# Performance work log

Hardware: AMD Instinct MI355X
Metric: run time of the kernel (lower is better)

## Reference

```python
import jax, jax.numpy as jnp
import numpy as np

D_MODEL = 1024
N_HEADS = 16
D_K = D_MODEL // N_HEADS

def setup_inputs() -> dict:
    key = jax.random.key(0)
    ks = jax.random.split(key, 9)
    s = 1.0 / np.sqrt(D_MODEL)
    inp = {"x": jax.random.normal(ks[0], (2, 2048, D_MODEL), dtype=jnp.float32)}
    for i, name in enumerate(["q", "k", "v", "o"]):
        inp[f"W{name}"] = jax.random.uniform(ks[1 + i], (D_MODEL, D_MODEL), dtype=jnp.float32, minval=-s, maxval=s)
        inp[f"b{name}"] = jax.random.uniform(ks[5 + i], (D_MODEL,), dtype=jnp.float32, minval=-s, maxval=s)
    return inp

def _split_heads(t):
    B, S, _ = t.shape
    return t.reshape(B, S, N_HEADS, D_K).transpose(0, 2, 1, 3)  # [B,H,S,d_k]

def reference(x, Wq, bq, Wk, bk, Wv, bv, Wo, bo):
    # QKV projections (torch Linear: x @ W.T + b)
    q = _split_heads(x @ Wq.T + bq)
    k = _split_heads(x @ Wk.T + bk)
    v = _split_heads(x @ Wv.T + bv)
    scores = jnp.einsum('bhqd,bhkd->bhqk', q, k) / jnp.sqrt(jnp.asarray(D_K, x.dtype))
    probs = jax.nn.softmax(scores, axis=-1)
    attn = jnp.einsum('bhqk,bhkd->bhqd', probs, v)  # [B,H,S,d_k]
    B, H, S, _ = attn.shape
    merged = attn.transpose(0, 2, 1, 3).reshape(B, S, D_MODEL)
    return merged @ Wo.T + bo
```

## Files before the change

kernel.cpp:

```cpp
#include <hip/hip_runtime.h>
#include <hip/hip_bf16.h>
#include <stdint.h>


#define LOG2E 1.4426950408889634f

typedef float f32x4 __attribute__((ext_vector_type(4)));
typedef short bf16x8 __attribute__((ext_vector_type(8)));
typedef short bf16x4 __attribute__((ext_vector_type(4)));

__device__ __forceinline__ unsigned short f2bf(float f) {
  __hip_bfloat16 h = __float2bfloat16(f);
  return reinterpret_cast<unsigned short&>(h);
}

#define GLDS(g, l) __builtin_amdgcn_global_load_lds(                          \
    (const __attribute__((address_space(1))) void*)(g),                       \
    (__attribute__((address_space(3))) void*)(l), 16, 0, 0)

__global__ __launch_bounds__(256) void k_conv(const float* __restrict__ src,
                                              unsigned short* __restrict__ dst,
                                              int n4, float scale) {
  int i = blockIdx.x * 256 + threadIdx.x;
  const int stride = gridDim.x * 256;
  for (; i < n4; i += stride) {
    float4 v = ((const float4*)src)[i];
    ushort4 o;
    o.x = f2bf(v.x * scale);
    o.y = f2bf(v.y * scale);
    o.z = f2bf(v.z * scale);
    o.w = f2bf(v.w * scale);
    ((ushort4*)dst)[i] = o;
  }
}

__global__ __launch_bounds__(256) void k_convW(const float* __restrict__ wq,
                                               const float* __restrict__ wk,
                                               const float* __restrict__ wv,
                                               const float* __restrict__ wo,
                                               unsigned short* __restrict__ dq,
                                               unsigned short* __restrict__ dk,
                                               unsigned short* __restrict__ dv,
                                               unsigned short* __restrict__ dw) {
  const int m = blockIdx.y;
  const float* src = (m == 0) ? wq : (m == 1) ? wk : (m == 2) ? wv : wo;
  unsigned short* dst = (m == 0) ? dq : (m == 1) ? dk : (m == 2) ? dv : dw;
  const float scale = (m == 0) ? (0.125f * LOG2E) : 1.0f;
  int i = blockIdx.x * 256 + threadIdx.x;
  float4 v = ((const float4*)src)[i];
  ushort4 o;
  o.x = f2bf(v.x * scale);
  o.y = f2bf(v.y * scale);
  o.z = f2bf(v.z * scale);
  o.w = f2bf(v.w * scale);
  ((ushort4*)dst)[i] = o;
}

__global__ __launch_bounds__(256) void k_bias(const float* __restrict__ bq,
                                              const float* __restrict__ bk,
                                              const float* __restrict__ bv,
                                              float* __restrict__ out) {
  int i = blockIdx.x * 256 + threadIdx.x;
  float v;
  if (i < 1024) v = bq[i] * (0.125f * LOG2E);
  else if (i < 2048) v = bk[i - 1024];
  else v = bv[i - 2048];
  out[i] = v;
}

template <int MODE>
__global__ __launch_bounds__(256) void k_gemm(const unsigned short* __restrict__ A,
                                              const unsigned short* __restrict__ B,
                                              const float* __restrict__ bias,
                                              void* __restrict__ outp) {
  __shared__ unsigned short As[128 * 32];
  __shared__ unsigned short Bs[128 * 32];
  const int tid = threadIdx.x;
  const int lane = tid & 63, wid = tid >> 6;
  const int wr = wid >> 1, wc = wid & 1;
  const int r = lane & 15, g = lane >> 4;
  const int bm = blockIdx.x, bn = blockIdx.y;

  const unsigned short* gA = A + (size_t)bm * 128 * 1024;
  const unsigned short* gB = B + (size_t)bn * 128 * 1024;
  const int row0 = tid >> 2, cg = (tid & 3) * 8;

  f32x4 acc[4][4] = {};

  for (int k0 = 0; k0 < 1024; k0 += 32) {
    __syncthreads();
    GLDS(gA + (size_t)row0 * 1024 + k0 + cg,        As + row0 * 32 + cg);
    GLDS(gA + (size_t)(row0 + 64) * 1024 + k0 + cg, As + (row0 + 64) * 32 + cg);
    GLDS(gB + (size_t)row0 * 1024 + k0 + cg,        Bs + row0 * 32 + cg);
    GLDS(gB + (size_t)(row0 + 64) * 1024 + k0 + cg, Bs + (row0 + 64) * 32 + cg);
    __syncthreads();

    bf16x8 af[4], bfr[4];
#pragma unroll
    for (int i = 0; i < 4; i++) {
      af[i]  = *(const bf16x8*)(As + (wr * 64 + i * 16 + r) * 32 + g * 8);
      bfr[i] = *(const bf16x8*)(Bs + (wc * 64 + i * 16 + r) * 32 + g * 8);
    }
#pragma unroll
    for (int i = 0; i < 4; i++)
#pragma unroll
      for (int j = 0; j < 4; j++)
        acc[i][j] = __builtin_amdgcn_mfma_f32_16x16x32_bf16(af[i], bfr[j], acc[i][j], 0, 0, 0);
  }

#pragma unroll
  for (int i = 0; i < 4; i++) {
    const int rowb = bm * 128 + wr * 64 + i * 16 + g * 4;
#pragma unroll
    for (int j = 0; j < 4; j++) {
      const int col = bn * 128 + wc * 64 + j * 16 + r;
      const float bv = bias[col];
#pragma unroll
      for (int t = 0; t < 4; t++) {
        const int row = rowb + t;
        const float val = acc[i][j][t] + bv;
        if (MODE == 0) {
          const int mat = col >> 10, nn = col & 1023;
          const int hh = nn >> 6, dd = nn & 63;
          const int bb = row >> 11, ss = row & 2047;
          size_t idx;
          if (mat == 2)
            idx = (size_t)2 * 4194304 + (size_t)((bb * 16 + hh) * 64 + dd) * 2048 + ss;
          else
            idx = (size_t)mat * 4194304 + (size_t)((bb * 16 + hh) * 2048 + ss) * 64 + dd;
          ((unsigned short*)outp)[idx] = f2bf(val);
        } else {
          ((float*)outp)[(size_t)row * 1024 + col] = val;
        }
      }
    }
  }
}

__global__ __launch_bounds__(256) void k_attn(const unsigned short* __restrict__ Q,
                                              const unsigned short* __restrict__ Km,
                                              const unsigned short* __restrict__ Vt,
                                              unsigned short* __restrict__ merged) {
  __shared__ unsigned short Kb[2][4096];
  __shared__ unsigned short Vb[2][4096];
  __shared__ unsigned short Pl[4][1024];
  const int tid = threadIdx.x;
  const int lane = tid & 63, w = tid >> 6;
  const int r = lane & 15, g = lane >> 4;
  const int bh = blockIdx.y;
  const int b = bh >> 4, h = bh & 15;
  const int q0 = blockIdx.x * 64;

  const unsigned short* Qh  = Q  + (size_t)bh * 131072;
  const unsigned short* Kh  = Km + (size_t)bh * 131072;
  const unsigned short* Vth = Vt + (size_t)bh * 131072;

  const int qrow = q0 + w * 16 + r;
  const bf16x8 bQ0 = *(const bf16x8*)(Qh + (size_t)qrow * 64 + g * 8);
  const bf16x8 bQ1 = *(const bf16x8*)(Qh + (size_t)qrow * 64 + 32 + g * 8);

  int ksrc[2], vsrc[2];
#pragma unroll
  for (int op = 0; op < 2; op++) {
    const int c = op * 256 + tid;
    const int st = c >> 7, dh = (c >> 6) & 1, gg = (c >> 4) & 3, rr = c & 15;
    ksrc[op] = (st * 16 + rr) * 64 + dh * 32 + gg * 8;
    vsrc[op] = (st * 16 + rr) * 2048 + dh * 32 + gg * 8;
  }
  const int ldst = tid * 8;

  GLDS(Kh + ksrc[0],  &Kb[0][ldst]);
  GLDS(Kh + ksrc[1],  &Kb[0][2048 + ldst]);
  GLDS(Vth + vsrc[0], &Vb[0][ldst]);
  GLDS(Vth + vsrc[1], &Vb[0][2048 + ldst]);
  __syncthreads();

  f32x4 o[4] = {};
  f32x4 ol = {};
  bf16x8 aONE;
#pragma unroll
  for (int j = 0; j < 8; j++) aONE[j] = (short)0x3F80;

  const unsigned swz = ((unsigned)(r & 7)) << 4;
  char* const plw = (char*)&Pl[w][0];

  for (int t = 0; t < 32; ++t) {
    const int cur = t & 1;
    if (t < 31) {
      const size_t kv = (size_t)(t + 1) * 64;
      GLDS(Kh + kv * 64 + ksrc[0],  &Kb[cur ^ 1][ldst]);
      GLDS(Kh + kv * 64 + ksrc[1],  &Kb[cur ^ 1][2048 + ldst]);
      GLDS(Vth + kv + vsrc[0], &Vb[cur ^ 1][ldst]);
      GLDS(Vth + kv + vsrc[1], &Vb[cur ^ 1][2048 + ldst]);
    }

    const unsigned short* kb = &Kb[cur][lane * 8];
    const unsigned short* vb = &Vb[cur][lane * 8];

    f32x4 St[4];
#pragma unroll
    for (int st = 0; st < 4; st++) {
      const bf16x8 a0 = *(const bf16x8*)(kb + st * 1024);
      const bf16x8 a1 = *(const bf16x8*)(kb + st * 1024 + 512);
      f32x4 z = {0.f, 0.f, 0.f, 0.f};
      z = __builtin_amdgcn_mfma_f32_16x16x32_bf16(a0, bQ0, z, 0, 0, 0);
      St[st] = __builtin_amdgcn_mfma_f32_16x16x32_bf16(a1, bQ1, z, 0, 0, 0);
    }

#pragma unroll
    for (int st = 0; st < 4; st++) {
      bf16x4 pk;
#pragma unroll
      for (int u = 0; u < 4; u++) pk[u] = (short)f2bf(exp2f(St[st][u]));
      *(bf16x4*)(plw + (((unsigned)(r * 128 + st * 32 + g * 8)) ^ swz)) = pk;
    }
    const bf16x8 pb0 = *(const bf16x8*)(plw + (((unsigned)(r * 128 + g * 16)) ^ swz));
    const bf16x8 pb1 = *(const bf16x8*)(plw + (((unsigned)(r * 128 + 64 + g * 16)) ^ swz));

#pragma unroll
    for (int c4 = 0; c4 < 4; c4++) {
      const bf16x8 v0 = *(const bf16x8*)(vb + c4 * 1024);
      const bf16x8 v1 = *(const bf16x8*)(vb + c4 * 1024 + 512);
      o[c4] = __builtin_amdgcn_mfma_f32_16x16x32_bf16(v0, pb0, o[c4], 0, 0, 0);
      o[c4] = __builtin_amdgcn_mfma_f32_16x16x32_bf16(v1, pb1, o[c4], 0, 0, 0);
    }
    ol = __builtin_amdgcn_mfma_f32_16x16x32_bf16(aONE, pb0, ol, 0, 0, 0);
    ol = __builtin_amdgcn_mfma_f32_16x16x32_bf16(aONE, pb1, ol, 0, 0, 0);

    __syncthreads();
  }

  const float inv = 1.0f / ol[0];
  const size_t base = (size_t)(b * 2048 + qrow) * 1024 + h * 64;
#pragma unroll
  for (int c4 = 0; c4 < 4; c4++)
#pragma unroll
    for (int u = 0; u < 4; u++)
      merged[base + c4 * 16 + g * 4 + u] = f2bf(o[c4][u] * inv);
}

extern "C" void kernel_launch(void* const* d_in, const int* in_sizes, int n_in,
                              void* d_out, int out_size, void* d_ws, size_t ws_size,
                              hipStream_t stream) {
  const float* x  = (const float*)d_in[0];
  const float* Wq = (const float*)d_in[1];
  const float* bq = (const float*)d_in[2];
  const float* Wk = (const float*)d_in[3];
  const float* bk = (const float*)d_in[4];
  const float* Wv = (const float*)d_in[5];
  const float* bv = (const float*)d_in[6];
  const float* Wo = (const float*)d_in[7];
  const float* bo = (const float*)d_in[8];

  if (ws_size < (size_t)50343936) return;

  unsigned short* ws  = (unsigned short*)d_ws;
  unsigned short* xb  = ws;
  unsigned short* Wb  = ws + 4194304;
  unsigned short* Wob = ws + 7340032;
  unsigned short* qkv = ws + 8388608;
  unsigned short* mrg = ws + 20971520;
  float* biasQ = (float*)(ws + 25165824);

  k_conv<<<dim3(2048), dim3(256), 0, stream>>>(x, xb, 1048576, 1.0f);
  k_convW<<<dim3(1024, 4), dim3(256), 0, stream>>>(Wq, Wk, Wv, Wo,
      Wb, Wb + 1048576, Wb + 2097152, Wob);
  k_bias<<<dim3(12), dim3(256), 0, stream>>>(bq, bk, bv, biasQ);

  k_gemm<0><<<dim3(32, 24), dim3(256), 0, stream>>>(xb, Wb, biasQ, (void*)qkv);
  k_attn<<<dim3(32, 32), dim3(256), 0, stream>>>(qkv, qkv + 4194304, qkv + 8388608, mrg);
  k_gemm<1><<<dim3(32, 8), dim3(256), 0, stream>>>(mrg, Wob, bo, d_out);
}
```

Measured before the change: 144.0 us.

## Double-buffer GEMM LDS tiles and process two query tiles per attention wave

```diff
diff --git a/kernel.cpp b/kernel.cpp
--- a/kernel.cpp
+++ b/kernel.cpp
@@ -73,8 +73,8 @@
                                               const unsigned short* __restrict__ B,
                                               const float* __restrict__ bias,
                                               void* __restrict__ outp) {
-  __shared__ unsigned short As[128 * 32];
-  __shared__ unsigned short Bs[128 * 32];
+  __shared__ unsigned short As[2][4096];
+  __shared__ unsigned short Bs[2][4096];
   const int tid = threadIdx.x;
   const int lane = tid & 63, wid = tid >> 6;
   const int wr = wid >> 1, wc = wid & 1;
@@ -87,25 +87,35 @@
 
   f32x4 acc[4][4] = {};
 
-  for (int k0 = 0; k0 < 1024; k0 += 32) {
-    __syncthreads();
-    GLDS(gA + (size_t)row0 * 1024 + k0 + cg,        As + row0 * 32 + cg);
-    GLDS(gA + (size_t)(row0 + 64) * 1024 + k0 + cg, As + (row0 + 64) * 32 + cg);
-    GLDS(gB + (size_t)row0 * 1024 + k0 + cg,        Bs + row0 * 32 + cg);
-    GLDS(gB + (size_t)(row0 + 64) * 1024 + k0 + cg, Bs + (row0 + 64) * 32 + cg);
-    __syncthreads();
+  GLDS(gA + (size_t)row0 * 1024 + cg,        &As[0][row0 * 32 + cg]);
+  GLDS(gA + (size_t)(row0 + 64) * 1024 + cg, &As[0][(row0 + 64) * 32 + cg]);
+  GLDS(gB + (size_t)row0 * 1024 + cg,        &Bs[0][row0 * 32 + cg]);
+  GLDS(gB + (size_t)(row0 + 64) * 1024 + cg, &Bs[0][(row0 + 64) * 32 + cg]);
+  __syncthreads();
+
+  for (int it = 0; it < 32; ++it) {
+    const int cur = it & 1;
+    if (it < 31) {
+      const int k0 = (it + 1) * 32;
+      GLDS(gA + (size_t)row0 * 1024 + k0 + cg,        &As[cur ^ 1][row0 * 32 + cg]);
+      GLDS(gA + (size_t)(row0 + 64) * 1024 + k0 + cg, &As[cur ^ 1][(row0 + 64) * 32 + cg]);
+      GLDS(gB + (size_t)row0 * 1024 + k0 + cg,        &Bs[cur ^ 1][row0 * 32 + cg]);
+      GLDS(gB + (size_t)(row0 + 64) * 1024 + k0 + cg, &Bs[cur ^ 1][(row0 + 64) * 32 + cg]);
+    }
 
     bf16x8 af[4], bfr[4];
 #pragma unroll
     for (int i = 0; i < 4; i++) {
-      af[i]  = *(const bf16x8*)(As + (wr * 64 + i * 16 + r) * 32 + g * 8);
-      bfr[i] = *(const bf16x8*)(Bs + (wc * 64 + i * 16 + r) * 32 + g * 8);
+      af[i]  = *(const bf16x8*)(&As[cur][(wr * 64 + i * 16 + r) * 32 + g * 8]);
+      bfr[i] = *(const bf16x8*)(&Bs[cur][(wc * 64 + i * 16 + r) * 32 + g * 8]);
     }
 #pragma unroll
     for (int i = 0; i < 4; i++)
 #pragma unroll
       for (int j = 0; j < 4; j++)
         acc[i][j] = __builtin_amdgcn_mfma_f32_16x16x32_bf16(af[i], bfr[j], acc[i][j], 0, 0, 0);
+
+    __syncthreads();
   }
 
 #pragma unroll
@@ -149,15 +159,19 @@
   const int r = lane & 15, g = lane >> 4;
   const int bh = blockIdx.y;
   const int b = bh >> 4, h = bh & 15;
-  const int q0 = blockIdx.x * 64;
+  const int q0 = blockIdx.x * 128;
 
   const unsigned short* Qh  = Q  + (size_t)bh * 131072;
   const unsigned short* Kh  = Km + (size_t)bh * 131072;
   const unsigned short* Vth = Vt + (size_t)bh * 131072;
 
-  const int qrow = q0 + w * 16 + r;
-  const bf16x8 bQ0 = *(const bf16x8*)(Qh + (size_t)qrow * 64 + g * 8);
-  const bf16x8 bQ1 = *(const bf16x8*)(Qh + (size_t)qrow * 64 + 32 + g * 8);
+  const int qrowA = q0 + w * 32 + r;
+  bf16x8 bQ[2][2];
+#pragma unroll
+  for (int f = 0; f < 2; f++) {
+    bQ[f][0] = *(const bf16x8*)(Qh + (size_t)(qrowA + f * 16) * 64 + g * 8);
+    bQ[f][1] = *(const bf16x8*)(Qh + (size_t)(qrowA + f * 16) * 64 + 32 + g * 8);
+  }
 
   int ksrc[2], vsrc[2];
 #pragma unroll
@@ -175,8 +189,8 @@
   GLDS(Vth + vsrc[1], &Vb[0][2048 + ldst]);
   __syncthreads();
 
-  f32x4 o[4] = {};
-  f32x4 ol = {};
+  f32x4 o[2][4] = {};
+  f32x4 ol[2] = {};
   bf16x8 aONE;
 #pragma unroll
   for (int j = 0; j < 8; j++) aONE[j] = (short)0x3F80;
@@ -197,46 +211,58 @@
     const unsigned short* kb = &Kb[cur][lane * 8];
     const unsigned short* vb = &Vb[cur][lane * 8];
 
-    f32x4 St[4];
+    bf16x8 kf[4][2], vf[4][2];
 #pragma unroll
     for (int st = 0; st < 4; st++) {
-      const bf16x8 a0 = *(const bf16x8*)(kb + st * 1024);
-      const bf16x8 a1 = *(const bf16x8*)(kb + st * 1024 + 512);
-      f32x4 z = {0.f, 0.f, 0.f, 0.f};
-      z = __builtin_amdgcn_mfma_f32_16x16x32_bf16(a0, bQ0, z, 0, 0, 0);
-      St[st] = __builtin_amdgcn_mfma_f32_16x16x32_bf16(a1, bQ1, z, 0, 0, 0);
-    }
-
-#pragma unroll
-    for (int st = 0; st < 4; st++) {
-      bf16x4 pk;
-#pragma unroll
-      for (int u = 0; u < 4; u++) pk[u] = (short)f2bf(exp2f(St[st][u]));
-      *(bf16x4*)(plw + (((unsigned)(r * 128 + st * 32 + g * 8)) ^ swz)) = pk;
-    }
-    const bf16x8 pb0 = *(const bf16x8*)(plw + (((unsigned)(r * 128 + g * 16)) ^ swz));
-    const bf16x8 pb1 = *(const bf16x8*)(plw + (((unsigned)(r * 128 + 64 + g * 16)) ^ swz));
-
-#pragma unroll
-    for (int c4 = 0; c4 < 4; c4++) {
-      const bf16x8 v0 = *(const bf16x8*)(vb + c4 * 1024);
-      const bf16x8 v1 = *(const bf16x8*)(vb + c4 * 1024 + 512);
-      o[c4] = __builtin_amdgcn_mfma_f32_16x16x32_bf16(v0, pb0, o[c4], 0, 0, 0);
-      o[c4] = __builtin_amdgcn_mfma_f32_16x16x32_bf16(v1, pb1, o[c4], 0, 0, 0);
-    }
-    ol = __builtin_amdgcn_mfma_f32_16x16x32_bf16(aONE, pb0, ol, 0, 0, 0);
-    ol = __builtin_amdgcn_mfma_f32_16x16x32_bf16(aONE, pb1, ol, 0, 0, 0);
+      kf[st][0] = *(const bf16x8*)(kb + st * 1024);
+      kf[st][1] = *(const bf16x8*)(kb + st * 1024 + 512);
+      vf[st][0] = *(const bf16x8*)(vb + st * 1024);
+      vf[st][1] = *(const bf16x8*)(vb + st * 1024 + 512);
+    }
+
+#pragma unroll
+    for (int f = 0; f < 2; f++) {
+      f32x4 St[4];
+#pragma unroll
+      for (int st = 0; st < 4; st++) {
+        f32x4 z = {0.f, 0.f, 0.f, 0.f};
+        z = __builtin_amdgcn_mfma_f32_16x16x32_bf16(kf[st][0], bQ[f][0], z, 0, 0, 0);
+        St[st] = __builtin_amdgcn_mfma_f32_16x16x32_bf16(kf[st][1], bQ[f][1], St[st] = z, 0, 0, 0);
+      }
+
+#pragma unroll
+      for (int st = 0; st < 4; st++) {
+        bf16x4 pk;
+#pragma unroll
+        for (int u = 0; u < 4; u++)
+          pk[u] = (short)f2bf(__builtin_amdgcn_exp2f(St[st][u]));
+        *(bf16x4*)(plw + (((unsigned)(r * 128 + st * 32 + g * 8)) ^ swz)) = pk;
+      }
+      const bf16x8 pb0 = *(const bf16x8*)(plw + (((unsigned)(r * 128 + g * 16)) ^ swz));
+      const bf16x8 pb1 = *(const bf16x8*)(plw + (((unsigned)(r * 128 + 64 + g * 16)) ^ swz));
+
+#pragma unroll
+      for (int c4 = 0; c4 < 4; c4++) {
+        o[f][c4] = __builtin_amdgcn_mfma_f32_16x16x32_bf16(vf[c4][0], pb0, o[f][c4], 0, 0, 0);
+        o[f][c4] = __builtin_amdgcn_mfma_f32_16x16x32_bf16(vf[c4][1], pb1, o[f][c4], 0, 0, 0);
+      }
+      ol[f] = __builtin_amdgcn_mfma_f32_16x16x32_bf16(aONE, pb0, ol[f], 0, 0, 0);
+      ol[f] = __builtin_amdgcn_mfma_f32_16x16x32_bf16(aONE, pb1, ol[f], 0, 0, 0);
+    }
 
     __syncthreads();
   }
 
-  const float inv = 1.0f / ol[0];
-  const size_t base = (size_t)(b * 2048 + qrow) * 1024 + h * 64;
-#pragma unroll
-  for (int c4 = 0; c4 < 4; c4++)
-#pragma unroll
-    for (int u = 0; u < 4; u++)
-      merged[base + c4 * 16 + g * 4 + u] = f2bf(o[c4][u] * inv);
+#pragma unroll
+  for (int f = 0; f < 2; f++) {
+    const float inv = 1.0f / ol[f][0];
+    const size_t base = (size_t)(b * 2048 + qrowA + f * 16) * 1024 + h * 64;
+#pragma unroll
+    for (int c4 = 0; c4 < 4; c4++)
+#pragma unroll
+      for (int u = 0; u < 4; u++)
+        merged[base + c4 * 16 + g * 4 + u] = f2bf(o[f][c4][u] * inv);
+  }
 }
 
 extern "C" void kernel_launch(void* const* d_in, const int* in_sizes, int n_in,
@@ -268,6 +294,6 @@
   k_bias<<<dim3(12), dim3(256), 0, stream>>>(bq, bk, bv, biasQ);
 
   k_gemm<0><<<dim3(32, 24), dim3(256), 0, stream>>>(xb, Wb, biasQ, (void*)qkv);
-  k_attn<<<dim3(32, 32), dim3(256), 0, stream>>>(qkv, qkv + 4194304, qkv + 8388608, mrg);
+  k_attn<<<dim3(16, 32), dim3(256), 0, stream>>>(qkv, qkv + 4194304, qkv + 8388608, mrg);
   k_gemm<1><<<dim3(32, 8), dim3(256), 0, stream>>>(mrg, Wob, bo, d_out);
 }
```

Result: faster. 139.9 us (-2.9%).

## Rewrite attention with 32x32 MFMA and register-resident P via permlane32 swap

Applied to the files above, without the earlier changes.

```diff
diff --git a/kernel.cpp b/kernel.cpp
--- a/kernel.cpp
+++ b/kernel.cpp
@@ -6,8 +6,10 @@
 #define LOG2E 1.4426950408889634f
 
 typedef float f32x4 __attribute__((ext_vector_type(4)));
+typedef float f32x16 __attribute__((ext_vector_type(16)));
 typedef short bf16x8 __attribute__((ext_vector_type(8)));
 typedef short bf16x4 __attribute__((ext_vector_type(4)));
+typedef unsigned int u32x2 __attribute__((ext_vector_type(2)));
 
 __device__ __forceinline__ unsigned short f2bf(float f) {
   __hip_bfloat16 h = __float2bfloat16(f);
@@ -143,29 +145,30 @@
                                               unsigned short* __restrict__ merged) {
   __shared__ unsigned short Kb[2][4096];
   __shared__ unsigned short Vb[2][4096];
-  __shared__ unsigned short Pl[4][1024];
   const int tid = threadIdx.x;
   const int lane = tid & 63, w = tid >> 6;
-  const int r = lane & 15, g = lane >> 4;
+  const int l31 = lane & 31, hi = lane >> 5;
   const int bh = blockIdx.y;
   const int b = bh >> 4, h = bh & 15;
-  const int q0 = blockIdx.x * 64;
+  const int q0 = blockIdx.x * 128;
 
   const unsigned short* Qh  = Q  + (size_t)bh * 131072;
   const unsigned short* Kh  = Km + (size_t)bh * 131072;
   const unsigned short* Vth = Vt + (size_t)bh * 131072;
 
-  const int qrow = q0 + w * 16 + r;
-  const bf16x8 bQ0 = *(const bf16x8*)(Qh + (size_t)qrow * 64 + g * 8);
-  const bf16x8 bQ1 = *(const bf16x8*)(Qh + (size_t)qrow * 64 + 32 + g * 8);
+  const int qrow = q0 + w * 32 + l31;
+  bf16x8 bQ[4];
+#pragma unroll
+  for (int c = 0; c < 4; c++)
+    bQ[c] = *(const bf16x8*)(Qh + (size_t)qrow * 64 + c * 16 + hi * 8);
 
   int ksrc[2], vsrc[2];
 #pragma unroll
   for (int op = 0; op < 2; op++) {
-    const int c = op * 256 + tid;
-    const int st = c >> 7, dh = (c >> 6) & 1, gg = (c >> 4) & 3, rr = c & 15;
-    ksrc[op] = (st * 16 + rr) * 64 + dh * 32 + gg * 8;
-    vsrc[op] = (st * 16 + rr) * 2048 + dh * 32 + gg * 8;
+    const int ck = op * 256 + tid;
+    const int s = ck >> 8, c = (ck >> 6) & 3, l2 = ck & 63;
+    ksrc[op] = (s * 32 + (l2 & 31)) * 64 + c * 16 + (l2 >> 5) * 8;
+    vsrc[op] = (s * 32 + (l2 & 31)) * 2048 + c * 16 + (l2 >> 5) * 8;
   }
   const int ldst = tid * 8;
 
@@ -175,14 +178,9 @@
   GLDS(Vth + vsrc[1], &Vb[0][2048 + ldst]);
   __syncthreads();
 
-  f32x4 o[4] = {};
-  f32x4 ol = {};
-  bf16x8 aONE;
-#pragma unroll
-  for (int j = 0; j < 8; j++) aONE[j] = (short)0x3F80;
-
-  const unsigned swz = ((unsigned)(r & 7)) << 4;
-  char* const plw = (char*)&Pl[w][0];
+  f32x16 o0 = {0.f,0.f,0.f,0.f,0.f,0.f,0.f,0.f,0.f,0.f,0.f,0.f,0.f,0.f,0.f,0.f};
+  f32x16 o1 = o0;
+  float lsum = 0.f;
 
   for (int t = 0; t < 32; ++t) {
     const int cur = t & 1;
@@ -194,49 +192,66 @@
       GLDS(Vth + kv + vsrc[1], &Vb[cur ^ 1][2048 + ldst]);
     }
 
-    const unsigned short* kb = &Kb[cur][lane * 8];
-    const unsigned short* vb = &Vb[cur][lane * 8];
-
-    f32x4 St[4];
-#pragma unroll
-    for (int st = 0; st < 4; st++) {
-      const bf16x8 a0 = *(const bf16x8*)(kb + st * 1024);
-      const bf16x8 a1 = *(const bf16x8*)(kb + st * 1024 + 512);
-      f32x4 z = {0.f, 0.f, 0.f, 0.f};
-      z = __builtin_amdgcn_mfma_f32_16x16x32_bf16(a0, bQ0, z, 0, 0, 0);
-      St[st] = __builtin_amdgcn_mfma_f32_16x16x32_bf16(a1, bQ1, z, 0, 0, 0);
-    }
-
-#pragma unroll
-    for (int st = 0; st < 4; st++) {
-      bf16x4 pk;
-#pragma unroll
-      for (int u = 0; u < 4; u++) pk[u] = (short)f2bf(exp2f(St[st][u]));
-      *(bf16x4*)(plw + (((unsigned)(r * 128 + st * 32 + g * 8)) ^ swz)) = pk;
-    }
-    const bf16x8 pb0 = *(const bf16x8*)(plw + (((unsigned)(r * 128 + g * 16)) ^ swz));
-    const bf16x8 pb1 = *(const bf16x8*)(plw + (((unsigned)(r * 128 + 64 + g * 16)) ^ swz));
-
-#pragma unroll
-    for (int c4 = 0; c4 < 4; c4++) {
-      const bf16x8 v0 = *(const bf16x8*)(vb + c4 * 1024);
-      const bf16x8 v1 = *(const bf16x8*)(vb + c4 * 1024 + 512);
-      o[c4] = __builtin_amdgcn_mfma_f32_16x16x32_bf16(v0, pb0, o[c4], 0, 0, 0);
-      o[c4] = __builtin_amdgcn_mfma_f32_16x16x32_bf16(v1, pb1, o[c4], 0, 0, 0);
-    }
-    ol = __builtin_amdgcn_mfma_f32_16x16x32_bf16(aONE, pb0, ol, 0, 0, 0);
-    ol = __builtin_amdgcn_mfma_f32_16x16x32_bf16(aONE, pb1, ol, 0, 0, 0);
+    bf16x8 kf[2][4], vf[2][4];
+#pragma unroll
+    for (int s = 0; s < 2; s++)
+#pragma unroll
+      for (int c = 0; c < 4; c++) {
+        kf[s][c] = *(const bf16x8*)(&Kb[cur][((s * 4 + c) * 64 + lane) * 8]);
+        vf[s][c] = *(const bf16x8*)(&Vb[cur][((s * 4 + c) * 64 + lane) * 8]);
+      }
+
+    f32x16 z = {0.f,0.f,0.f,0.f,0.f,0.f,0.f,0.f,0.f,0.f,0.f,0.f,0.f,0.f,0.f,0.f};
+    f32x16 St0 = z, St1 = z;
+#pragma unroll
+    for (int c = 0; c < 4; c++) {
+      St0 = __builtin_amdgcn_mfma_f32_32x32x16_bf16(kf[0][c], bQ[c], St0, 0, 0, 0);
+      St1 = __builtin_amdgcn_mfma_f32_32x32x16_bf16(kf[1][c], bQ[c], St1, 0, 0, 0);
+    }
+
+    float p0[16], p1[16];
+    float ps = 0.f;
+#pragma unroll
+    for (int u = 0; u < 16; u++) {
+      p0[u] = __builtin_amdgcn_exp2f(St0[u]);
+      p1[u] = __builtin_amdgcn_exp2f(St1[u]);
+      ps += p0[u] + p1[u];
+    }
+    lsum += ps;
+
+#pragma unroll
+    for (int c = 0; c < 4; c++) {
+      const float* pp = (c < 2) ? p0 : p1;
+      const int R = (c & 1) * 8;
+      unsigned int a0, a1, b0, b1;
+      asm("v_cvt_pk_bf16_f32 %0, %1, %2" : "=v"(a0) : "v"(pp[R + 0]), "v"(pp[R + 1]));
+      asm("v_cvt_pk_bf16_f32 %0, %1, %2" : "=v"(a1) : "v"(pp[R + 2]), "v"(pp[R + 3]));
+      asm("v_cvt_pk_bf16_f32 %0, %1, %2" : "=v"(b0) : "v"(pp[R + 4]), "v"(pp[R + 5]));
+      asm("v_cvt_pk_bf16_f32 %0, %1, %2" : "=v"(b1) : "v"(pp[R + 6]), "v"(pp[R + 7]));
+      u32x2 r0 = __builtin_amdgcn_permlane32_swap(a0, b0, false, false);
+      u32x2 r1 = __builtin_amdgcn_permlane32_swap(a1, b1, false, false);
+      union { unsigned int u[4]; bf16x8 v; } pf;
+      pf.u[0] = r0[0]; pf.u[1] = r1[0]; pf.u[2] = r0[1]; pf.u[3] = r1[1];
+      o0 = __builtin_amdgcn_mfma_f32_32x32x16_bf16(vf[0][c], pf.v, o0, 0, 0, 0);
+      o1 = __builtin_amdgcn_mfma_f32_32x32x16_bf16(vf[1][c], pf.v, o1, 0, 0, 0);
+    }
 
     __syncthreads();
   }
 
-  const float inv = 1.0f / ol[0];
+  const float inv = 1.0f / (lsum + __shfl_xor(lsum, 32));
   const size_t base = (size_t)(b * 2048 + qrow) * 1024 + h * 64;
 #pragma unroll
-  for (int c4 = 0; c4 < 4; c4++)
-#pragma unroll
-    for (int u = 0; u < 4; u++)
-      merged[base + c4 * 16 + g * 4 + u] = f2bf(o[c4][u] * inv);
+  for (int ds = 0; ds < 2; ds++) {
+    const f32x16& oo = ds ? o1 : o0;
+#pragma unroll
+    for (int m = 0; m < 4; m++) {
+      bf16x4 ov;
+#pragma unroll
+      for (int i = 0; i < 4; i++) ov[i] = (short)f2bf(oo[m * 4 + i] * inv);
+      *(bf16x4*)(&merged[base + ds * 32 + m * 8 + hi * 4]) = ov;
+    }
+  }
 }
 
 extern "C" void kernel_launch(void* const* d_in, const int* in_sizes, int n_in,
@@ -268,6 +283,6 @@
   k_bias<<<dim3(12), dim3(256), 0, stream>>>(bq, bk, bv, biasQ);
 
   k_gemm<0><<<dim3(32, 24), dim3(256), 0, stream>>>(xb, Wb, biasQ, (void*)qkv);
-  k_attn<<<dim3(32, 32), dim3(256), 0, stream>>>(qkv, qkv + 4194304, qkv + 8388608, mrg);
+  k_attn<<<dim3(16, 32), dim3(256), 0, stream>>>(qkv, qkv + 4194304, qkv + 8388608, mrg);
   k_gemm<1><<<dim3(32, 8), dim3(256), 0, stream>>>(mrg, Wob, bo, d_out);
 }
```

Result: faster. 134.0 us (-7.0%).
